# Kernel tuning notes

Measured on AMD Instinct MI355X. Metric: run time of the kernel, lower is better.

Reference implementation:

```python
import jax, jax.numpy as jnp
import numpy as np

M, K, N, R = 8192, 4096, 4096, 32
GROUP = 64  # nunchaku W4A4 quantization group size
QMAX = 7.0  # int4 symmetric


def setup_inputs() -> dict:
    key = jax.random.key(0)
    ks = jax.random.split(key, 6)
    x = jax.random.normal(ks[0], (M, K), dtype=jnp.float32)
    w_res = jax.random.normal(ks[1], (N, K), dtype=jnp.float32) * 0.02
    lora_down = jax.random.normal(ks[2], (K, R), dtype=jnp.float32) * 0.02
    lora_up = jax.random.normal(ks[3], (N, R), dtype=jnp.float32) * 0.02
    smooth = 0.5 + jax.random.uniform(ks[4], (K,), dtype=jnp.float32)  # positive 1/s factors
    b = jax.random.normal(ks[5], (N,), dtype=jnp.float32)
    return {"x": x, "w_res": w_res, "lora_down": lora_down, "lora_up": lora_up, "smooth": smooth, "b": b}


def _fake_quant_int4(t, group):
    # symmetric int4 fake-quant with per-group absmax scales along last dim
    shp = t.shape
    tg = t.reshape(shp[:-1] + (shp[-1] // group, group))
    scale = jnp.maximum(jnp.max(jnp.abs(tg), axis=-1, keepdims=True) / QMAX, 1e-8)
    q = jnp.clip(jnp.round(tg / scale), -8.0, 7.0) * scale
    return q.reshape(shp)


def reference(x, w_res, lora_down, lora_up, smooth, b):
    # smoothed activation (smooth = 1/s applied by kernel before quantization)
    xs = x * smooth[None, :]                       # [M, K]
    xq = _fake_quant_int4(xs, GROUP)               # per-token per-group int4
    wq = _fake_quant_int4(w_res, GROUP)            # per-outchannel per-group int4
    # W4A4 GEMM on dequantized values + fused low-rank LoRA correction + bias
    main = jnp.einsum('mk,nk->mn', xq, wq)         # [M, N]
    lora = jnp.einsum('mr,nr->mn', xs @ lora_down, lora_up)
    return main + lora + b[None, :]
```

## Files before the change

kernel.cpp:

```cpp
#include <hip/hip_runtime.h>
#include <hip/hip_bf16.h>
#include <stdint.h>

#define M_DIM 8192
#define N_DIM 4096
#define K_DIM 4096
#define R_DIM 32
#define KPAD  4160
#define NT    65
#define QMAXF 7.0f

using bf16_t = __hip_bfloat16;
typedef __attribute__((ext_vector_type(4))) float f32x4;
typedef __attribute__((ext_vector_type(8))) short bf16x8;

__device__ __forceinline__ void stage16(const void* g, void* l) {
#if defined(__has_builtin) && __has_builtin(__builtin_amdgcn_global_load_lds)
  __builtin_amdgcn_global_load_lds(
      (const __attribute__((address_space(1))) unsigned int*)g,
      (__attribute__((address_space(3))) unsigned int*)l, 16, 0, 0);
#else
  *(uint4*)l = *(const uint4*)g;
#endif
}

__global__ __launch_bounds__(256) void quant_x_kernel(
    const float* __restrict__ x, const float* __restrict__ smooth,
    bf16_t* __restrict__ Ap) {
  const int row = blockIdx.x;
  const int tid = threadIdx.x;
  const int k0  = tid * 16;
  const float* xr = x + (size_t)row * K_DIM + k0;
  const float* sr = smooth + k0;

  float v[16];
#pragma unroll
  for (int i = 0; i < 4; ++i) {
    float4 xv = *(const float4*)(xr + i * 4);
    float4 sv = *(const float4*)(sr + i * 4);
    v[i*4+0] = xv.x * sv.x; v[i*4+1] = xv.y * sv.y;
    v[i*4+2] = xv.z * sv.z; v[i*4+3] = xv.w * sv.w;
  }
  float am = 0.f;
#pragma unroll
  for (int i = 0; i < 16; ++i) am = fmaxf(am, fabsf(v[i]));
  am = fmaxf(am, __shfl_xor(am, 1));
  am = fmaxf(am, __shfl_xor(am, 2));
  const float scale = fmaxf(am / QMAXF, 1e-8f);

  alignas(16) bf16_t o[16];
#pragma unroll
  for (int i = 0; i < 16; ++i) {
    float q = rintf(v[i] / scale);
    q = fminf(fmaxf(q, -8.f), 7.f);
    o[i] = __float2bfloat16(q * scale);
  }
  bf16_t* dst = Ap + (size_t)row * KPAD + k0;
  ((uint4*)dst)[0] = ((uint4*)o)[0];
  ((uint4*)dst)[1] = ((uint4*)o)[1];

  if (tid < 32) Ap[(size_t)row * KPAD + 4128 + tid] = __float2bfloat16(0.f);
}

__global__ __launch_bounds__(256) void quant_w_kernel(
    const float* __restrict__ w, const float* __restrict__ lora_up,
    bf16_t* __restrict__ Bp) {
  const int row = blockIdx.x;
  const int tid = threadIdx.x;
  const int k0  = tid * 16;
  const float* wr = w + (size_t)row * K_DIM + k0;

  float v[16];
#pragma unroll
  for (int i = 0; i < 4; ++i) {
    float4 wv = *(const float4*)(wr + i * 4);
    v[i*4+0] = wv.x; v[i*4+1] = wv.y; v[i*4+2] = wv.z; v[i*4+3] = wv.w;
  }
  float am = 0.f;
#pragma unroll
  for (int i = 0; i < 16; ++i) am = fmaxf(am, fabsf(v[i]));
  am = fmaxf(am, __shfl_xor(am, 1));
  am = fmaxf(am, __shfl_xor(am, 2));
  const float scale = fmaxf(am / QMAXF, 1e-8f);

  alignas(16) bf16_t o[16];
#pragma unroll
  for (int i = 0; i < 16; ++i) {
    float q = rintf(v[i] / scale);
    q = fminf(fmaxf(q, -8.f), 7.f);
    o[i] = __float2bfloat16(q * scale);
  }
  bf16_t* dst = Bp + (size_t)row * KPAD + k0;
  ((uint4*)dst)[0] = ((uint4*)o)[0];
  ((uint4*)dst)[1] = ((uint4*)o)[1];

  if (tid < 32) {
    Bp[(size_t)row * KPAD + 4096 + tid] = __float2bfloat16(lora_up[row * R_DIM + tid]);
  } else if (tid < 64) {
    Bp[(size_t)row * KPAD + 4096 + tid] = __float2bfloat16(0.f);
  }
}

__global__ __launch_bounds__(256) void ldT_kernel(
    const float* __restrict__ ld, bf16_t* __restrict__ ldT) {
  const int k = blockIdx.x * 256 + threadIdx.x;
  float v[R_DIM];
#pragma unroll
  for (int i = 0; i < R_DIM / 4; ++i) {
    float4 a = *(const float4*)(ld + (size_t)k * R_DIM + i * 4);
    v[i*4+0] = a.x; v[i*4+1] = a.y; v[i*4+2] = a.z; v[i*4+3] = a.w;
  }
#pragma unroll
  for (int r = 0; r < R_DIM; ++r)
    ldT[(size_t)r * K_DIM + k] = __float2bfloat16(v[r]);
}

__global__ __launch_bounds__(256) void lora_mfma_kernel(
    const float* __restrict__ x, const float* __restrict__ smooth,
    const bf16_t* __restrict__ ldT, bf16_t* __restrict__ Ap) {
  const int tid  = threadIdx.x;
  const int w    = tid >> 6;
  const int lane = tid & 63;
  const int m0   = blockIdx.x * 32;

  const int mrow = m0 + (w >> 1) * 16 + (lane & 15);
  const int ncol = (w & 1) * 16 + (lane & 15);
  const float* xr = x + (size_t)mrow * K_DIM;
  const bf16_t* br = ldT + (size_t)ncol * K_DIM;

  f32x4 acc = {0.f, 0.f, 0.f, 0.f};
  union { bf16_t h[8]; bf16x8 v; } au;

  for (int k = 0; k < K_DIM; k += 32) {
    const int kf = k + (lane >> 4) * 8;
    float4 x0 = *(const float4*)(xr + kf);
    float4 x1 = *(const float4*)(xr + kf + 4);
    float4 s0 = *(const float4*)(smooth + kf);
    float4 s1 = *(const float4*)(smooth + kf + 4);
    au.h[0] = __float2bfloat16(x0.x * s0.x);
    au.h[1] = __float2bfloat16(x0.y * s0.y);
    au.h[2] = __float2bfloat16(x0.z * s0.z);
    au.h[3] = __float2bfloat16(x0.w * s0.w);
    au.h[4] = __float2bfloat16(x1.x * s1.x);
    au.h[5] = __float2bfloat16(x1.y * s1.y);
    au.h[6] = __float2bfloat16(x1.z * s1.z);
    au.h[7] = __float2bfloat16(x1.w * s1.w);
    bf16x8 bv = *(const bf16x8*)(br + kf);
    acc = __builtin_amdgcn_mfma_f32_16x16x32_bf16(au.v, bv, acc, 0, 0, 0);
  }

  const int orow = m0 + (w >> 1) * 16 + (lane >> 4) * 4;
  const int ocol = 4096 + ncol;
#pragma unroll
  for (int q = 0; q < 4; ++q)
    Ap[(size_t)(orow + q) * KPAD + ocol] = __float2bfloat16(acc[q]);
}

__global__ __launch_bounds__(512, 2) void gemm_kernel(
    const bf16_t* __restrict__ A, const bf16_t* __restrict__ B,
    const float* __restrict__ bias, float* __restrict__ C) {
  extern __shared__ __align__(16) bf16_t lds[];

  const int wg  = blockIdx.x;
  const int swz = (wg & 7) * 64 + (wg >> 3);
  const int bn  = swz & 15;
  const int bm  = swz >> 4;

  const int tid  = threadIdx.x;
  const int lane = tid & 63;
  const int wid  = tid >> 6;
  const int wm   = wid >> 2;
  const int wn   = wid & 3;

  const int lr = lane & 15;
  const int lg = lane >> 4;
  const int l7 = lane & 7;
  const int gk0 = ((0 + lg) ^ l7) * 8;
  const int gk1 = ((4 + lg) ^ l7) * 8;

  const int sr   = tid >> 3;
  const int sl   = tid & 7;
  const int gcol = (sl ^ (sr & 7)) * 8;
  const bf16_t* Abase = A + (size_t)(bm * 256 + ((sr >> 5) & 1) * 128 + (sr & 31)) * KPAD + gcol;
  const bf16_t* Bbase = B + (size_t)(bn * 256 + sr) * KPAD + gcol;
  bf16_t* ldsb = lds;

#define STAGE_A(buf, h, kt) do {                                               \
    stage16(Abase + (size_t)((h) * 2 + 0) * 32 * KPAD + (kt) * 64,             \
            ldsb + (buf) * 32768 + (h) * 8192 + 0 * 4096 + tid * 8);           \
    stage16(Abase + (size_t)((h) * 2 + 1) * 32 * KPAD + (kt) * 64,             \
            ldsb + (buf) * 32768 + (h) * 8192 + 1 * 4096 + tid * 8);           \
  } while (0)
#define STAGE_B(buf, h, kt) do {                                               \
    stage16(Bbase + (size_t)((h) * 128 + 0) * KPAD + (kt) * 64,                \
            ldsb + (buf) * 32768 + 16384 + (h) * 8192 + 0 * 4096 + tid * 8);   \
    stage16(Bbase + (size_t)((h) * 128 + 64) * KPAD + (kt) * 64,               \
            ldsb + (buf) * 32768 + 16384 + (h) * 8192 + 1 * 4096 + tid * 8);   \
  } while (0)

  f32x4  acc[8][4] = {};
  bf16x8 aF[2][2];
  bf16x8 bA[4][2];
  bf16x8 bB[4][2];

#define LOAD_A(q, cur) do {                                                    \
    const bf16_t* pa_ = ldsb + (cur) * 32768 + ((q) * 64 + wm * 32 + lr) * 64; \
    aF[0][0] = *(const bf16x8*)(pa_ + gk0);                                    \
    aF[0][1] = *(const bf16x8*)(pa_ + gk1);                                    \
    aF[1][0] = *(const bf16x8*)(pa_ + 1024 + gk0);                             \
    aF[1][1] = *(const bf16x8*)(pa_ + 1024 + gk1);                             \
  } while (0)
#define LOAD_BN(BN, nbuf) do {                                                 \
    _Pragma("unroll")                                                          \
    for (int j = 0; j < 4; ++j) {                                              \
      const bf16_t* pb_ = ldsb + (nbuf) * 32768 + 16384 + (wn * 64 + j * 16 + lr) * 64; \
      BN[j][0] = *(const bf16x8*)(pb_ + gk0);                                  \
      BN[j][1] = *(const bf16x8*)(pb_ + gk1);                                  \
    }                                                                          \
  } while (0)
#define MFMA_Q(q, BARR) do {                                                   \
    _Pragma("unroll")                                                          \
    for (int i = 0; i < 2; ++i)                                                \
      _Pragma("unroll")                                                        \
      for (int j = 0; j < 4; ++j) {                                            \
        acc[(q)*2+i][j] = __builtin_amdgcn_mfma_f32_16x16x32_bf16(             \
            aF[i][0], BARR[j][0], acc[(q)*2+i][j], 0, 0, 0);                   \
        acc[(q)*2+i][j] = __builtin_amdgcn_mfma_f32_16x16x32_bf16(             \
            aF[i][1], BARR[j][1], acc[(q)*2+i][j], 0, 0, 0);                   \
      }                                                                        \
  } while (0)
#define TAIL_PLAIN(q, BARR) do {                                               \
    __builtin_amdgcn_s_barrier();                                              \
    asm volatile("s_waitcnt lgkmcnt(0)" ::: "memory");                         \
    __builtin_amdgcn_s_setprio(1);                                             \
    MFMA_Q(q, BARR);                                                           \
    __builtin_amdgcn_s_setprio(0);                                             \
    __builtin_amdgcn_s_barrier();                                              \
  } while (0)

#define KTILE(u, cur, BCUR, BNXT) do {                                         \
    LOAD_A(0, cur);                                                            \
    if ((u) + 1 < NT) STAGE_A((cur) ^ 1, 1, (u) + 1);                          \
    TAIL_PLAIN(0, BCUR);                                                       \
    LOAD_A(1, cur);                                                            \
    if ((u) + 2 < NT) STAGE_B(cur, 0, (u) + 2);                                \
    TAIL_PLAIN(1, BCUR);                                                       \
    LOAD_A(2, cur);                                                            \
    if ((u) + 2 < NT) STAGE_B(cur, 1, (u) + 2);                                \
    TAIL_PLAIN(2, BCUR);                                                       \
    LOAD_A(3, cur);                                                            \
    if ((u) + 2 < NT) {                                                        \
      STAGE_A(cur, 0, (u) + 2);                                                \
      asm volatile("s_waitcnt vmcnt(6)" ::: "memory");                         \
    } else {                                                                   \
      asm volatile("s_waitcnt vmcnt(0)" ::: "memory");                         \
    }                                                                          \
    __builtin_amdgcn_s_barrier();                                              \
    asm volatile("s_waitcnt lgkmcnt(0)" ::: "memory");                         \
    if ((u) + 1 < NT) LOAD_BN(BNXT, (cur) ^ 1);                                \
    __builtin_amdgcn_s_setprio(1);                                             \
    MFMA_Q(3, BCUR);                                                           \
    __builtin_amdgcn_s_setprio(0);                                             \
    __builtin_amdgcn_s_barrier();                                              \
  } while (0)

  STAGE_B(0, 0, 0); STAGE_B(0, 1, 0); STAGE_A(0, 0, 0); STAGE_A(0, 1, 0);
  STAGE_B(1, 0, 1); STAGE_B(1, 1, 1); STAGE_A(1, 0, 1);
  asm volatile("s_waitcnt vmcnt(6)" ::: "memory");
  __builtin_amdgcn_s_barrier();
  LOAD_BN(bA, 0);

  for (int base = 0; base < 64; base += 2) {
    KTILE(base,     0, bA, bB);
    KTILE(base + 1, 1, bB, bA);
  }
  KTILE(64, 0, bA, bB);

  const int colb = bn * 256 + wn * 64 + lr;
  const int rowb = bm * 256 + wm * 128 + lg * 4;
#pragma unroll
  for (int j = 0; j < 4; ++j) {
    const int gc = colb + j * 16;
    const float bv = bias[gc];
#pragma unroll
    for (int q = 0; q < 4; ++q)
#pragma unroll
      for (int i = 0; i < 2; ++i) {
        const int gr = rowb + q * 32 + i * 16;
#pragma unroll
        for (int e = 0; e < 4; ++e)
          C[(size_t)(gr + e) * N_DIM + gc] = acc[q * 2 + i][j][e] + bv;
      }
  }
#undef STAGE_A
#undef STAGE_B
#undef LOAD_A
#undef LOAD_BN
#undef MFMA_Q
#undef TAIL_PLAIN
#undef KTILE
}

extern "C" void kernel_launch(void* const* d_in, const int* in_sizes, int n_in,
                              void* d_out, int out_size, void* d_ws, size_t ws_size,
                              hipStream_t stream) {
  const float* x         = (const float*)d_in[0];
  const float* w_res     = (const float*)d_in[1];
  const float* lora_down = (const float*)d_in[2];
  const float* lora_up   = (const float*)d_in[3];
  const float* smooth    = (const float*)d_in[4];
  const float* b         = (const float*)d_in[5];
  float* out = (float*)d_out;

  bf16_t* Ap  = (bf16_t*)d_ws;
  bf16_t* Bp  = Ap + (size_t)M_DIM * KPAD;
  bf16_t* ldT = Bp + (size_t)N_DIM * KPAD;

  hipFuncSetAttribute((const void*)gemm_kernel,
                      hipFuncAttributeMaxDynamicSharedMemorySize, 131072);

  quant_x_kernel<<<M_DIM, 256, 0, stream>>>(x, smooth, Ap);
  quant_w_kernel<<<N_DIM, 256, 0, stream>>>(w_res, lora_up, Bp);
  ldT_kernel<<<K_DIM / 256, 256, 0, stream>>>(lora_down, ldT);
  lora_mfma_kernel<<<M_DIM / 32, 256, 0, stream>>>(x, smooth, ldT, Ap);
  gemm_kernel<<<(M_DIM / 256) * (N_DIM / 256), 512, 131072, stream>>>(Ap, Bp, b, out);
}
```

Baseline: 366.7 us.

## Merge prep kernels and double-buffer A fragments in GEMM k-tile pipeline

Measured after the change: 358.2 us, median of 2. 2.3% less time.

```diff
diff --git a/kernel.cpp b/kernel.cpp
--- a/kernel.cpp
+++ b/kernel.cpp
@@ -24,95 +24,94 @@
 #endif
 }
 
-__global__ __launch_bounds__(256) void quant_x_kernel(
+__global__ __launch_bounds__(256) void prep_kernel(
     const float* __restrict__ x, const float* __restrict__ smooth,
-    bf16_t* __restrict__ Ap) {
-  const int row = blockIdx.x;
+    const float* __restrict__ w, const float* __restrict__ lora_up,
+    const float* __restrict__ ld,
+    bf16_t* __restrict__ Ap, bf16_t* __restrict__ Bp,
+    bf16_t* __restrict__ ldT) {
+  const int bid = blockIdx.x;
   const int tid = threadIdx.x;
-  const int k0  = tid * 16;
-  const float* xr = x + (size_t)row * K_DIM + k0;
-  const float* sr = smooth + k0;
-
-  float v[16];
-#pragma unroll
-  for (int i = 0; i < 4; ++i) {
-    float4 xv = *(const float4*)(xr + i * 4);
-    float4 sv = *(const float4*)(sr + i * 4);
-    v[i*4+0] = xv.x * sv.x; v[i*4+1] = xv.y * sv.y;
-    v[i*4+2] = xv.z * sv.z; v[i*4+3] = xv.w * sv.w;
+
+  if (bid < M_DIM) {
+    const int row = bid;
+    const int k0  = tid * 16;
+    const float* xr = x + (size_t)row * K_DIM + k0;
+    const float* sr = smooth + k0;
+
+    float v[16];
+#pragma unroll
+    for (int i = 0; i < 4; ++i) {
+      float4 xv = *(const float4*)(xr + i * 4);
+      float4 sv = *(const float4*)(sr + i * 4);
+      v[i*4+0] = xv.x * sv.x; v[i*4+1] = xv.y * sv.y;
+      v[i*4+2] = xv.z * sv.z; v[i*4+3] = xv.w * sv.w;
+    }
+    float am = 0.f;
+#pragma unroll
+    for (int i = 0; i < 16; ++i) am = fmaxf(am, fabsf(v[i]));
+    am = fmaxf(am, __shfl_xor(am, 1));
+    am = fmaxf(am, __shfl_xor(am, 2));
+    const float scale = fmaxf(am / QMAXF, 1e-8f);
+
+    alignas(16) bf16_t o[16];
+#pragma unroll
+    for (int i = 0; i < 16; ++i) {
+      float q = rintf(v[i] / scale);
+      q = fminf(fmaxf(q, -8.f), 7.f);
+      o[i] = __float2bfloat16(q * scale);
+    }
+    bf16_t* dst = Ap + (size_t)row * KPAD + k0;
+    ((uint4*)dst)[0] = ((uint4*)o)[0];
+    ((uint4*)dst)[1] = ((uint4*)o)[1];
+    if (tid < 32) Ap[(size_t)row * KPAD + 4128 + tid] = __float2bfloat16(0.f);
+
+  } else if (bid < M_DIM + N_DIM) {
+    const int row = bid - M_DIM;
+    const int k0  = tid * 16;
+    const float* wr = w + (size_t)row * K_DIM + k0;
+
+    float v[16];
+#pragma unroll
+    for (int i = 0; i < 4; ++i) {
+      float4 wv = *(const float4*)(wr + i * 4);
+      v[i*4+0] = wv.x; v[i*4+1] = wv.y; v[i*4+2] = wv.z; v[i*4+3] = wv.w;
+    }
+    float am = 0.f;
+#pragma unroll
+    for (int i = 0; i < 16; ++i) am = fmaxf(am, fabsf(v[i]));
+    am = fmaxf(am, __shfl_xor(am, 1));
+    am = fmaxf(am, __shfl_xor(am, 2));
+    const float scale = fmaxf(am / QMAXF, 1e-8f);
+
+    alignas(16) bf16_t o[16];
+#pragma unroll
+    for (int i = 0; i < 16; ++i) {
+      float q = rintf(v[i] / scale);
+      q = fminf(fmaxf(q, -8.f), 7.f);
+      o[i] = __float2bfloat16(q * scale);
+    }
+    bf16_t* dst = Bp + (size_t)row * KPAD + k0;
+    ((uint4*)dst)[0] = ((uint4*)o)[0];
+    ((uint4*)dst)[1] = ((uint4*)o)[1];
+    if (tid < 32) {
+      Bp[(size_t)row * KPAD + 4096 + tid] = __float2bfloat16(lora_up[row * R_DIM + tid]);
+    } else if (tid < 64) {
+      Bp[(size_t)row * KPAD + 4096 + tid] = __float2bfloat16(0.f);
+    }
+
+  } else {
+    const int k = (bid - M_DIM - N_DIM) * 256 + tid;
+    float v[R_DIM];
+#pragma unroll
+    for (int i = 0; i < R_DIM / 4; ++i) {
+      float4 a = *(const float4*)(ld + (size_t)k * R_DIM + i * 4);
+      v[i*4+0] = a.x; v[i*4+1] = a.y; v[i*4+2] = a.z; v[i*4+3] = a.w;
+    }
+#pragma unroll
+    for (int r = 0; r < R_DIM; ++r)
+      ldT[(size_t)r * K_DIM + k] = __float2bfloat16(v[r]);
   }
-  float am = 0.f;
-#pragma unroll
-  for (int i = 0; i < 16; ++i) am = fmaxf(am, fabsf(v[i]));
-  am = fmaxf(am, __shfl_xor(am, 1));
-  am = fmaxf(am, __shfl_xor(am, 2));
-  const float scale = fmaxf(am / QMAXF, 1e-8f);
-
-  alignas(16) bf16_t o[16];
-#pragma unroll
-  for (int i = 0; i < 16; ++i) {
-    float q = rintf(v[i] / scale);
-    q = fminf(fmaxf(q, -8.f), 7.f);
-    o[i] = __float2bfloat16(q * scale);
-  }
-  bf16_t* dst = Ap + (size_t)row * KPAD + k0;
-  ((uint4*)dst)[0] = ((uint4*)o)[0];
-  ((uint4*)dst)[1] = ((uint4*)o)[1];
-
-  if (tid < 32) Ap[(size_t)row * KPAD + 4128 + tid] = __float2bfloat16(0.f);
-}
-
-__global__ __launch_bounds__(256) void quant_w_kernel(
-    const float* __restrict__ w, const float* __restrict__ lora_up,
-    bf16_t* __restrict__ Bp) {
-  const int row = blockIdx.x;
-  const int tid = threadIdx.x;
-  const int k0  = tid * 16;
-  const float* wr = w + (size_t)row * K_DIM + k0;
-
-  float v[16];
-#pragma unroll
-  for (int i = 0; i < 4; ++i) {
-    float4 wv = *(const float4*)(wr + i * 4);
-    v[i*4+0] = wv.x; v[i*4+1] = wv.y; v[i*4+2] = wv.z; v[i*4+3] = wv.w;
-  }
-  float am = 0.f;
-#pragma unroll
-  for (int i = 0; i < 16; ++i) am = fmaxf(am, fabsf(v[i]));
-  am = fmaxf(am, __shfl_xor(am, 1));
-  am = fmaxf(am, __shfl_xor(am, 2));
-  const float scale = fmaxf(am / QMAXF, 1e-8f);
-
-  alignas(16) bf16_t o[16];
-#pragma unroll
-  for (int i = 0; i < 16; ++i) {
-    float q = rintf(v[i] / scale);
-    q = fminf(fmaxf(q, -8.f), 7.f);
-    o[i] = __float2bfloat16(q * scale);
-  }
-  bf16_t* dst = Bp + (size_t)row * KPAD + k0;
-  ((uint4*)dst)[0] = ((uint4*)o)[0];
-  ((uint4*)dst)[1] = ((uint4*)o)[1];
-
-  if (tid < 32) {
-    Bp[(size_t)row * KPAD + 4096 + tid] = __float2bfloat16(lora_up[row * R_DIM + tid]);
-  } else if (tid < 64) {
-    Bp[(size_t)row * KPAD + 4096 + tid] = __float2bfloat16(0.f);
-  }
-}
-
-__global__ __launch_bounds__(256) void ldT_kernel(
-    const float* __restrict__ ld, bf16_t* __restrict__ ldT) {
-  const int k = blockIdx.x * 256 + threadIdx.x;
-  float v[R_DIM];
-#pragma unroll
-  for (int i = 0; i < R_DIM / 4; ++i) {
-    float4 a = *(const float4*)(ld + (size_t)k * R_DIM + i * 4);
-    v[i*4+0] = a.x; v[i*4+1] = a.y; v[i*4+2] = a.z; v[i*4+3] = a.w;
-  }
-#pragma unroll
-  for (int r = 0; r < R_DIM; ++r)
-    ldT[(size_t)r * K_DIM + k] = __float2bfloat16(v[r]);
 }
 
 __global__ __launch_bounds__(256) void lora_mfma_kernel(
@@ -199,56 +198,72 @@
   } while (0)
 
   f32x4  acc[8][4] = {};
-  bf16x8 aF[2][2];
-  bf16x8 bA[4][2];
-  bf16x8 bB[4][2];
-
-#define LOAD_A(q, cur) do {                                                    \
-    const bf16_t* pa_ = ldsb + (cur) * 32768 + ((q) * 64 + wm * 32 + lr) * 64; \
-    aF[0][0] = *(const bf16x8*)(pa_ + gk0);                                    \
-    aF[0][1] = *(const bf16x8*)(pa_ + gk1);                                    \
-    aF[1][0] = *(const bf16x8*)(pa_ + 1024 + gk0);                             \
-    aF[1][1] = *(const bf16x8*)(pa_ + 1024 + gk1);                             \
-  } while (0)
-#define LOAD_BN(BN, nbuf) do {                                                 \
+  bf16x8 aA[2][2];
+  bf16x8 aB[2][2];
+  bf16x8 bF[4][2];
+
+#define LOAD_A(DST, q, cb) do {                                                \
+    const bf16_t* pa_ = ldsb + (cb) * 32768 + ((q) * 64 + wm * 32 + lr) * 64;  \
+    DST[0][0] = *(const bf16x8*)(pa_ + gk0);                                   \
+    DST[0][1] = *(const bf16x8*)(pa_ + gk1);                                   \
+    DST[1][0] = *(const bf16x8*)(pa_ + 1024 + gk0);                            \
+    DST[1][1] = *(const bf16x8*)(pa_ + 1024 + gk1);                            \
+  } while (0)
+#define LOAD_BN(nbuf) do {                                                     \
     _Pragma("unroll")                                                          \
     for (int j = 0; j < 4; ++j) {                                              \
       const bf16_t* pb_ = ldsb + (nbuf) * 32768 + 16384 + (wn * 64 + j * 16 + lr) * 64; \
-      BN[j][0] = *(const bf16x8*)(pb_ + gk0);                                  \
-      BN[j][1] = *(const bf16x8*)(pb_ + gk1);                                  \
+      bF[j][0] = *(const bf16x8*)(pb_ + gk0);                                  \
+      bF[j][1] = *(const bf16x8*)(pb_ + gk1);                                  \
     }                                                                          \
   } while (0)
-#define MFMA_Q(q, BARR) do {                                                   \
+#define MFMA_Q(q, AARR) do {                                                   \
     _Pragma("unroll")                                                          \
     for (int i = 0; i < 2; ++i)                                                \
       _Pragma("unroll")                                                        \
       for (int j = 0; j < 4; ++j) {                                            \
         acc[(q)*2+i][j] = __builtin_amdgcn_mfma_f32_16x16x32_bf16(             \
-            aF[i][0], BARR[j][0], acc[(q)*2+i][j], 0, 0, 0);                   \
+            AARR[i][0], bF[j][0], acc[(q)*2+i][j], 0, 0, 0);                   \
         acc[(q)*2+i][j] = __builtin_amdgcn_mfma_f32_16x16x32_bf16(             \
-            aF[i][1], BARR[j][1], acc[(q)*2+i][j], 0, 0, 0);                   \
+            AARR[i][1], bF[j][1], acc[(q)*2+i][j], 0, 0, 0);                   \
       }                                                                        \
   } while (0)
-#define TAIL_PLAIN(q, BARR) do {                                               \
+
+#define KTILE(u, cur) do {                                                     \
+                                                             \
+    if ((u) + 1 < NT) STAGE_A((cur) ^ 1, 1, (u) + 1);                          \
     __builtin_amdgcn_s_barrier();                                              \
     asm volatile("s_waitcnt lgkmcnt(0)" ::: "memory");                         \
+    __builtin_amdgcn_sched_barrier(0);                                         \
+    LOAD_A(aB, 1, cur);                                                        \
+    __builtin_amdgcn_sched_barrier(0);                                         \
     __builtin_amdgcn_s_setprio(1);                                             \
-    MFMA_Q(q, BARR);                                                           \
+    MFMA_Q(0, aA);                                                             \
     __builtin_amdgcn_s_setprio(0);                                             \
     __builtin_amdgcn_s_barrier();                                              \
-  } while (0)
-
-#define KTILE(u, cur, BCUR, BNXT) do {                                         \
-    LOAD_A(0, cur);                                                            \
-    if ((u) + 1 < NT) STAGE_A((cur) ^ 1, 1, (u) + 1);                          \
-    TAIL_PLAIN(0, BCUR);                                                       \
-    LOAD_A(1, cur);                                                            \
+                                                             \
     if ((u) + 2 < NT) STAGE_B(cur, 0, (u) + 2);                                \
-    TAIL_PLAIN(1, BCUR);                                                       \
-    LOAD_A(2, cur);                                                            \
+    __builtin_amdgcn_s_barrier();                                              \
+    asm volatile("s_waitcnt lgkmcnt(0)" ::: "memory");                         \
+    __builtin_amdgcn_sched_barrier(0);                                         \
+    LOAD_A(aA, 2, cur);                                                        \
+    __builtin_amdgcn_sched_barrier(0);                                         \
+    __builtin_amdgcn_s_setprio(1);                                             \
+    MFMA_Q(1, aB);                                                             \
+    __builtin_amdgcn_s_setprio(0);                                             \
+    __builtin_amdgcn_s_barrier();                                              \
+                                                             \
     if ((u) + 2 < NT) STAGE_B(cur, 1, (u) + 2);                                \
-    TAIL_PLAIN(2, BCUR);                                                       \
-    LOAD_A(3, cur);                                                            \
+    __builtin_amdgcn_s_barrier();                                              \
+    asm volatile("s_waitcnt lgkmcnt(0)" ::: "memory");                         \
+    __builtin_amdgcn_sched_barrier(0);                                         \
+    LOAD_A(aB, 3, cur);                                                        \
+    __builtin_amdgcn_sched_barrier(0);                                         \
+    __builtin_amdgcn_s_setprio(1);                                             \
+    MFMA_Q(2, aA);                                                             \
+    __builtin_amdgcn_s_setprio(0);                                             \
+    __builtin_amdgcn_s_barrier();                                              \
+                                                             \
     if ((u) + 2 < NT) {                                                        \
       STAGE_A(cur, 0, (u) + 2);                                                \
       asm volatile("s_waitcnt vmcnt(6)" ::: "memory");                         \
@@ -257,10 +272,14 @@
     }                                                                          \
     __builtin_amdgcn_s_barrier();                                              \
     asm volatile("s_waitcnt lgkmcnt(0)" ::: "memory");                         \
-    if ((u) + 1 < NT) LOAD_BN(BNXT, (cur) ^ 1);                                \
+    __builtin_amdgcn_sched_barrier(0);                                         \
+    if ((u) + 1 < NT) LOAD_A(aA, 0, (cur) ^ 1);                                \
+    __builtin_amdgcn_sched_barrier(0);                                         \
     __builtin_amdgcn_s_setprio(1);                                             \
-    MFMA_Q(3, BCUR);                                                           \
+    MFMA_Q(3, aB);                                                             \
     __builtin_amdgcn_s_setprio(0);                                             \
+    __builtin_amdgcn_sched_barrier(0);                                         \
+    if ((u) + 1 < NT) LOAD_BN((cur) ^ 1);                                      \
     __builtin_amdgcn_s_barrier();                                              \
   } while (0)
 
@@ -268,13 +287,14 @@
   STAGE_B(1, 0, 1); STAGE_B(1, 1, 1); STAGE_A(1, 0, 1);
   asm volatile("s_waitcnt vmcnt(6)" ::: "memory");
   __builtin_amdgcn_s_barrier();
-  LOAD_BN(bA, 0);
+  LOAD_BN(0);
+  LOAD_A(aA, 0, 0);
 
   for (int base = 0; base < 64; base += 2) {
-    KTILE(base,     0, bA, bB);
-    KTILE(base + 1, 1, bB, bA);
+    KTILE(base,     0);
+    KTILE(base + 1, 1);
   }
-  KTILE(64, 0, bA, bB);
+  KTILE(64, 0);
 
   const int colb = bn * 256 + wn * 64 + lr;
   const int rowb = bm * 256 + wm * 128 + lg * 4;
@@ -297,7 +317,6 @@
 #undef LOAD_A
 #undef LOAD_BN
 #undef MFMA_Q
-#undef TAIL_PLAIN
 #undef KTILE
 }
 
@@ -319,9 +338,8 @@
   hipFuncSetAttribute((const void*)gemm_kernel,
                       hipFuncAttributeMaxDynamicSharedMemorySize, 131072);
 
-  quant_x_kernel<<<M_DIM, 256, 0, stream>>>(x, smooth, Ap);
-  quant_w_kernel<<<N_DIM, 256, 0, stream>>>(w_res, lora_up, Bp);
-  ldT_kernel<<<K_DIM / 256, 256, 0, stream>>>(lora_down, ldT);
+  prep_kernel<<<M_DIM + N_DIM + K_DIM / 256, 256, 0, stream>>>(
+      x, smooth, w_res, lora_up, lora_down, Ap, Bp, ldT);
   lora_mfma_kernel<<<M_DIM / 32, 256, 0, stream>>>(x, smooth, ldT, Ap);
   gemm_kernel<<<(M_DIM / 256) * (N_DIM / 256), 512, 131072, stream>>>(Ap, Bp, b, out);
 }
```
